# Performance work log

Measured on AMD Instinct MI355X. Metric: run time of the kernel, lower is better.

## Reference

```python
import jax, jax.numpy as jnp
import numpy as np

N_NODES = 100000
N_EDGES = 1600000
IN_DIM = 128
N_HID = 128


def setup_inputs() -> dict:
    key = jax.random.key(0)
    k1, k2, k3, k4 = jax.random.split(key, 4)
    node_feature = jax.random.normal(k1, (N_NODES, IN_DIM), dtype=jnp.float32)
    edge_index = jax.random.randint(k2, (2, N_EDGES), 0, N_NODES, dtype=jnp.int64)
    # GCN layer weights (glorot-ish scale)
    W1 = jax.random.normal(k3, (IN_DIM, N_HID), dtype=jnp.float32) / np.sqrt(IN_DIM)
    b1 = jnp.zeros((N_HID,), dtype=jnp.float32)
    W2 = jax.random.normal(k4, (N_HID, N_HID), dtype=jnp.float32) / np.sqrt(N_HID)
    b2 = jnp.zeros((N_HID,), dtype=jnp.float32)
    return {"node_feature": node_feature, "edge_index": edge_index,
            "W1": W1, "b1": b1, "W2": W2, "b2": b2}


def _gcn_layer(x, W, b, row, col, n_nodes):
    """GCNConv: x' = D^-1/2 (A + I) D^-1/2 (x W) + b, symmetric norm with self-loops."""
    xt = x @ W  # [N, out]
    ones = jnp.ones(row.shape[0], dtype=xt.dtype)
    deg = jnp.zeros((n_nodes,), dtype=xt.dtype).at[col].add(ones) + 1.0  # +1 self-loop
    dinv = jax.lax.rsqrt(deg)  # [N]
    norm = dinv[row] * dinv[col]  # [E]
    # gather messages from source (row), scatter-add into destination (col)
    agg = jnp.zeros_like(xt).at[col].add(xt[row] * norm[:, None])
    agg = agg + xt * (dinv * dinv)[:, None]  # self-loop contribution
    return agg + b


def reference(node_feature, edge_index, W1, b1, W2, b2):
    row, col = edge_index[0], edge_index[1]
    n = node_feature.shape[0]
    h = _gcn_layer(node_feature, W1, b1, row, col, n)
    # F.dropout with training=False is identity (eval-mode reference)
    h = _gcn_layer(h, W2, b2, row, col, n)
    return h
```

## Files before the change

kernel.cpp:

```cpp
#include <hip/hip_runtime.h>

typedef unsigned short ushort_t;
typedef __attribute__((ext_vector_type(8))) short short8;
typedef __attribute__((ext_vector_type(8))) unsigned short us8v;
typedef __attribute__((ext_vector_type(4))) float f32x4;

__device__ __forceinline__ float b2f(unsigned short u) {
    union { unsigned int i; float f; } v; v.i = ((unsigned int)u) << 16; return v.f;
}
__device__ __forceinline__ unsigned short f2b(float f) {
    union { float f; unsigned int i; } v; v.f = f;
    unsigned int r = (v.i + 0x7FFF + ((v.i >> 16) & 1)) >> 16;
    return (unsigned short)r;
}

__device__ __forceinline__ void load_edge(const int* __restrict__ ei, int e, int E,
                                          int is64, int& s, int& d) {
    if (is64) {
        const long long* el = (const long long*)ei;
        s = (int)el[e]; d = (int)el[E + e];
    } else {
        s = ei[e]; d = ei[E + e];
    }
}

__device__ __forceinline__ int detect64(const int* __restrict__ ei, int t) {
    int z = 0;
    for (int i = t; i < 512; i += 256) z |= ei[2 * i + 1];
    return (__syncthreads_or(z) == 0);
}

__global__ __launch_bounds__(256) void k_histT(const int* __restrict__ ei, int E,
                                               unsigned N, int* __restrict__ bhist,
                                               int BSH, int NB, int nch,
                                               const float* __restrict__ W1,
                                               const float* __restrict__ W2,
                                               ushort_t* __restrict__ WT) {
    __shared__ int lh[256];
    int t = threadIdx.x;
    int b = blockIdx.x;
    if (b >= nch) {
        const float* src = (b == nch) ? W1 : W2;
        ushort_t* dst = WT + (b - nch) * 16384;
        for (int i = t; i < 16384; i += 256) {
            int n = i >> 7, k = i & 127;
            dst[i] = f2b(src[k * 128 + n]);
        }
        return;
    }
    for (int q = t; q < NB; q += 256) lh[q] = 0;
    int is64 = detect64(ei, t);
    int e0 = b * 4096;
    #pragma unroll
    for (int i = 0; i < 16; ++i) {
        int e = e0 + i * 256 + t;
        if (e < E) {
            int s, d; load_edge(ei, e, E, is64, s, d);
            if ((unsigned)s < N && (unsigned)d < N) atomicAdd(&lh[d >> BSH], 1);
        }
    }
    __syncthreads();
    for (int q = t; q < NB; q += 256) { int v = lh[q]; if (v) atomicAdd(&bhist[q], v); }
}

__global__ void k_scanb(const int* __restrict__ bhist, int NB,
                        int* __restrict__ bkbase, int* __restrict__ bkcur) {
    __shared__ int sd[256];
    int t = threadIdx.x;
    int v0 = (t < NB) ? bhist[t] : 0;
    sd[t] = v0;
    for (int o = 1; o < 256; o <<= 1) {
        __syncthreads();
        int v = (t >= o) ? sd[t - o] : 0;
        __syncthreads();
        sd[t] += v;
    }
    __syncthreads();
    if (t < NB) { int ex = sd[t] - v0; bkbase[t] = ex; bkcur[t] = ex; }
}

__global__ __launch_bounds__(256) void k_bucket(const int* __restrict__ ei, int E, unsigned N,
                                                int* __restrict__ bkcur,
                                                int* __restrict__ bs, int* __restrict__ bd,
                                                int BSH, int NB) {
    __shared__ int lss[4096];
    __shared__ int ldd[4096];
    __shared__ int lhist[256];
    __shared__ int lcur[256];
    int t = threadIdx.x;
    int e0 = blockIdx.x * 4096;
    for (int b = t; b < NB; b += 256) lhist[b] = 0;
    int is64 = detect64(ei, t);
    #pragma unroll
    for (int i = 0; i < 16; ++i) {
        int idx = i * 256 + t, e = e0 + idx;
        int s = -1, d = -1;
        if (e < E) {
            load_edge(ei, e, E, is64, s, d);
            if (!((unsigned)s < N && (unsigned)d < N)) d = -1;
        }
        lss[idx] = s; ldd[idx] = d;
        if (d >= 0) atomicAdd(&lhist[d >> BSH], 1);
    }
    __syncthreads();
    for (int b = t; b < NB; b += 256) {
        int v = lhist[b];
        lcur[b] = v ? atomicAdd(&bkcur[b], v) : 0;
    }
    __syncthreads();
    #pragma unroll
    for (int i = 0; i < 16; ++i) {
        int idx = i * 256 + t;
        int d = ldd[idx];
        if (d >= 0) {
            int p = atomicAdd(&lcur[d >> BSH], 1);
            bs[p] = lss[idx]; bd[p] = d;
        }
    }
}

__global__ __launch_bounds__(256) void k_caf(const int* __restrict__ bs,
                                             const int* __restrict__ bd,
                                             const int* __restrict__ bkbase,
                                             const int* __restrict__ bkcur,
                                             int N, int BSH,
                                             int* __restrict__ pos,
                                             int* __restrict__ cnt,
                                             float* __restrict__ dinv,
                                             int* __restrict__ srcs) {
    __shared__ int lc[512];
    __shared__ int sc[512];
    int b = blockIdx.x, t = threadIdx.x;
    int nbase = b << BSH;
    int nn = min(1 << BSH, N - nbase);
    int segbase = bkbase[b] + b * (7 << BSH);

    lc[t] = 0; lc[t + 256] = 0;
    __syncthreads();
    int s0 = bkbase[b], s1 = bkcur[b];
    for (int i = s0 + t; i < s1; i += 256) atomicAdd(&lc[bd[i] - nbase], 1);
    __syncthreads();

    int c0 = (t < nn) ? lc[t] : 0;
    int c1 = (t + 256 < nn) ? lc[t + 256] : 0;
    int p0 = (c0 + 7) & ~7;
    int p1 = (c1 + 7) & ~7;
    sc[t] = p0; sc[t + 256] = p1;
    __syncthreads();
    for (int o = 1; o < 512; o <<= 1) {
        int v0 = (t >= o) ? sc[t - o] : 0;
        int v1 = (t + 256 >= o) ? sc[t + 256 - o] : 0;
        __syncthreads();
        sc[t] += v0; sc[t + 256] += v1;
        __syncthreads();
    }
    if (t < nn) {
        int st = segbase + sc[t] - p0;
        pos[nbase + t] = st;
        cnt[nbase + t] = p0;
        dinv[nbase + t] = rsqrtf((float)c0 + 1.0f);
        for (int q = c0; q < p0; ++q) srcs[st + q] = N;
        lc[t] = st;
    }
    if (t + 256 < nn) {
        int st = segbase + sc[t + 256] - p1;
        pos[nbase + t + 256] = st;
        cnt[nbase + t + 256] = p1;
        dinv[nbase + t + 256] = rsqrtf((float)c1 + 1.0f);
        for (int q = c1; q < p1; ++q) srcs[st + q] = N;
        lc[t + 256] = st;
    }
    __syncthreads();
    for (int i = s0 + t; i < s1; i += 256) {
        int d = bd[i];
        int p = atomicAdd(&lc[d - nbase], 1);
        srcs[p] = bs[i];
    }
}

template <bool ABF, bool ZROW>
__global__ __launch_bounds__(256) void k_gemm(const void* __restrict__ Ap,
                                              const ushort_t* __restrict__ WT,
                                              ushort_t* __restrict__ C,
                                              const float* __restrict__ dinv, int M) {
    __shared__ __align__(16) ushort_t sA[64 * 136];
    __shared__ __align__(16) ushort_t sW[128 * 136];
    int t = threadIdx.x;
    int row0 = blockIdx.x * 64;

    if (ZROW && blockIdx.x == 0 && t < 128) C[((size_t)M << 7) + t] = 0;

    #pragma unroll
    for (int it = 0; it < 8; ++it) {
        int flat = (it * 256 + t) * 8;
        int n = flat >> 7, k = flat & 127;
        uint4 v = *(const uint4*)(WT + flat);
        *(uint4*)(&sW[n * 136 + k]) = v;
    }
    #pragma unroll
    for (int it = 0; it < 4; ++it) {
        int flat = (it * 256 + t) * 8;
        int r = flat >> 7, cc = flat & 127;
        int row = row0 + r; if (row > M - 1) row = M - 1;
        if (ABF) {
            const ushort_t* A = (const ushort_t*)Ap;
            us8v v = *(const us8v*)(A + ((size_t)row << 7) + cc);
            *(us8v*)(&sA[r * 136 + cc]) = v;
        } else {
            const float* A = (const float*)Ap;
            const float* p = A + (size_t)row * 128 + cc;
            float4 f0 = *(const float4*)p;
            float4 f1 = *(const float4*)(p + 4);
            ushort_t tmp[8] __attribute__((aligned(16)));
            tmp[0] = f2b(f0.x); tmp[1] = f2b(f0.y); tmp[2] = f2b(f0.z); tmp[3] = f2b(f0.w);
            tmp[4] = f2b(f1.x); tmp[5] = f2b(f1.y); tmp[6] = f2b(f1.z); tmp[7] = f2b(f1.w);
            *(uint4*)(&sA[r * 136 + cc]) = *(const uint4*)tmp;
        }
    }
    __syncthreads();

    int w = t >> 6, lane = t & 63;
    int m = lane & 15, quad = lane >> 4;

    f32x4 acc[8] = {};
    #pragma unroll
    for (int k0 = 0; k0 < 128; k0 += 32) {
        short8 af = *(const short8*)(&sA[(w * 16 + m) * 136 + k0 + quad * 8]);
        #pragma unroll
        for (int tt = 0; tt < 8; ++tt) {
            short8 bf = *(const short8*)(&sW[(tt * 16 + m) * 136 + k0 + quad * 8]);
            acc[tt] = __builtin_amdgcn_mfma_f32_16x16x32_bf16(af, bf, acc[tt], 0, 0, 0);
        }
    }
    #pragma unroll
    for (int r = 0; r < 4; ++r) {
        int row = row0 + w * 16 + quad * 4 + r;
        if (row < M) {
            float dd = dinv[row];
            #pragma unroll
            for (int tt = 0; tt < 8; ++tt)
                C[(size_t)row * 128 + tt * 16 + m] = f2b(dd * acc[tt][r]);
        }
    }
}

template <bool OBF>
__global__ __launch_bounds__(256) void k_agg(const ushort_t* __restrict__ xt,
                                             const float* __restrict__ bias,
                                             void* __restrict__ outp,
                                             const int* __restrict__ pos,
                                             const int* __restrict__ cnts,
                                             const float* __restrict__ dinv,
                                             const int* __restrict__ srcs, int N) {
    int lane = threadIdx.x & 63;
    int slot = lane >> 4, j = lane & 15;
    int d = (blockIdx.x << 2) + (threadIdx.x >> 6);
    if (d >= N) return;
    int cn = cnts[d];
    int start = pos[d];
    float dd = dinv[d];
    us8v vs = *(const us8v*)(xt + ((size_t)d << 7) + (j << 3));
    float4 bb0 = *(const float4*)(bias + (j << 3));
    float4 bb1 = *(const float4*)(bias + (j << 3) + 4);

    float a0 = 0.f, a1 = 0.f, a2 = 0.f, a3 = 0.f;
    float a4 = 0.f, a5 = 0.f, a6 = 0.f, a7 = 0.f;

    for (int base = 0; base < cn; base += 64) {
        int n = cn - base; if (n > 64) n = 64;
        int sv = 0;
        if (lane < n) sv = srcs[start + base + lane];
        int s0 = __shfl(sv, slot);
        int s1 = __shfl(sv, 4 + slot);
        us8v v0 = *(const us8v*)(xt + ((size_t)s0 << 7) + (j << 3));
        us8v v1 = *(const us8v*)(xt + ((size_t)s1 << 7) + (j << 3));
        for (int c = 8; c < n; c += 8) {
            int t0 = __shfl(sv, c + slot);
            int t1 = __shfl(sv, c + 4 + slot);
            us8v w0 = *(const us8v*)(xt + ((size_t)t0 << 7) + (j << 3));
            us8v w1 = *(const us8v*)(xt + ((size_t)t1 << 7) + (j << 3));
            a0 += b2f(v0[0]); a1 += b2f(v0[1]); a2 += b2f(v0[2]); a3 += b2f(v0[3]);
            a4 += b2f(v0[4]); a5 += b2f(v0[5]); a6 += b2f(v0[6]); a7 += b2f(v0[7]);
            a0 += b2f(v1[0]); a1 += b2f(v1[1]); a2 += b2f(v1[2]); a3 += b2f(v1[3]);
            a4 += b2f(v1[4]); a5 += b2f(v1[5]); a6 += b2f(v1[6]); a7 += b2f(v1[7]);
            v0 = w0; v1 = w1;
        }
        a0 += b2f(v0[0]); a1 += b2f(v0[1]); a2 += b2f(v0[2]); a3 += b2f(v0[3]);
        a4 += b2f(v0[4]); a5 += b2f(v0[5]); a6 += b2f(v0[6]); a7 += b2f(v0[7]);
        a0 += b2f(v1[0]); a1 += b2f(v1[1]); a2 += b2f(v1[2]); a3 += b2f(v1[3]);
        a4 += b2f(v1[4]); a5 += b2f(v1[5]); a6 += b2f(v1[6]); a7 += b2f(v1[7]);
    }
    a0 += __shfl_xor(a0, 32); a1 += __shfl_xor(a1, 32);
    a2 += __shfl_xor(a2, 32); a3 += __shfl_xor(a3, 32);
    a4 += __shfl_xor(a4, 32); a5 += __shfl_xor(a5, 32);
    a6 += __shfl_xor(a6, 32); a7 += __shfl_xor(a7, 32);
    a0 += __shfl_xor(a0, 16); a1 += __shfl_xor(a1, 16);
    a2 += __shfl_xor(a2, 16); a3 += __shfl_xor(a3, 16);
    a4 += __shfl_xor(a4, 16); a5 += __shfl_xor(a5, 16);
    a6 += __shfl_xor(a6, 16); a7 += __shfl_xor(a7, 16);

    if (slot == 0) {
        float o0 = dd * (a0 + b2f(vs[0])) + bb0.x;
        float o1 = dd * (a1 + b2f(vs[1])) + bb0.y;
        float o2 = dd * (a2 + b2f(vs[2])) + bb0.z;
        float o3 = dd * (a3 + b2f(vs[3])) + bb0.w;
        float o4 = dd * (a4 + b2f(vs[4])) + bb1.x;
        float o5 = dd * (a5 + b2f(vs[5])) + bb1.y;
        float o6 = dd * (a6 + b2f(vs[6])) + bb1.z;
        float o7 = dd * (a7 + b2f(vs[7])) + bb1.w;
        if (OBF) {
            ushort_t tmp[8] __attribute__((aligned(16)));
            tmp[0] = f2b(o0); tmp[1] = f2b(o1); tmp[2] = f2b(o2); tmp[3] = f2b(o3);
            tmp[4] = f2b(o4); tmp[5] = f2b(o5); tmp[6] = f2b(o6); tmp[7] = f2b(o7);
            *(us8v*)((ushort_t*)outp + ((size_t)d << 7) + (j << 3)) = *(const us8v*)tmp;
        } else {
            float4 q0 = { o0, o1, o2, o3 };
            float4 q1 = { o4, o5, o6, o7 };
            float4* po = (float4*)((float*)outp + ((size_t)d << 7) + (j << 3));
            po[0] = q0; po[1] = q1;
        }
    }
}


extern "C" void kernel_launch(void* const* d_in, const int* in_sizes, int n_in,
                              void* d_out, int out_size, void* d_ws, size_t ws_size,
                              hipStream_t stream) {
    const float* x  = (const float*)d_in[0];
    const int*   ei = (const int*)d_in[1];
    const float* W1 = (const float*)d_in[2];
    const float* b1 = (const float*)d_in[3];
    const float* W2 = (const float*)d_in[4];
    const float* b2 = (const float*)d_in[5];
    float* out = (float*)d_out;

    const int N = in_sizes[0] / 128;
    const int E = in_sizes[1] / 2;

    int BSH = 9;
    int NB = (N + (1 << BSH) - 1) >> BSH;
    while (NB > 256) { BSH++; NB = (N + (1 << BSH) - 1) >> BSH; }

    char* ws = (char*)d_ws;
    size_t o = 0;
    auto take = [&](size_t bytes) { size_t r = o; o = (o + bytes + 255) & ~(size_t)255; return r; };
    size_t o_bhist  = take(256 * 4);
    size_t zero_end = o;
    size_t o_bkbase = take(256 * 4);
    size_t o_bkcur  = take(256 * 4);
    size_t o_cnt    = take((size_t)N * 4);
    size_t o_pos    = take((size_t)N * 4);
    size_t o_dinv   = take((size_t)N * 4);
    size_t o_srcs   = take(((size_t)E + (size_t)NB * (7 << BSH) + 64) * 4);
    size_t o_WT     = take(2 * 128 * 128 * 2);
    size_t big_sz   = (size_t)E * 8 > (size_t)(N + 1) * 256 ? (size_t)E * 8
                                                            : (size_t)(N + 1) * 256;
    size_t o_big    = take(big_sz);
    (void)ws_size;

    int*      bhist  = (int*)(ws + o_bhist);
    int*      bkbase = (int*)(ws + o_bkbase);
    int*      bkcur  = (int*)(ws + o_bkcur);
    int*      cnt    = (int*)(ws + o_cnt);
    int*      pos    = (int*)(ws + o_pos);
    float*    dinv   = (float*)(ws + o_dinv);
    int*      srcs   = (int*)(ws + o_srcs);
    ushort_t* WT     = (ushort_t*)(ws + o_WT);
    int*      bs     = (int*)(ws + o_big);
    int*      bd     = (int*)(ws + o_big) + E;
    ushort_t* xt     = (ushort_t*)(ws + o_big);
    ushort_t* hbf    = (ushort_t*)d_out;

    hipMemsetAsync(d_ws, 0, zero_end, stream);

    int nch = (E + 4095) / 4096;
    int gG  = (N + 63) / 64;
    int gA  = (N + 3) / 4;
    unsigned Nu = (unsigned)N;

    k_histT<<<nch + 2, 256, 0, stream>>>(ei, E, Nu, bhist, BSH, NB, nch, W1, W2, WT);
    k_scanb<<<1, 256, 0, stream>>>(bhist, NB, bkbase, bkcur);
    k_bucket<<<nch, 256, 0, stream>>>(ei, E, Nu, bkcur, bs, bd, BSH, NB);
    k_caf<<<NB, 256, 0, stream>>>(bs, bd, bkbase, bkcur, N, BSH, pos, cnt, dinv, srcs);

    k_gemm<false, true><<<gG, 256, 0, stream>>>(x, WT, xt, dinv, N);
    k_agg<true><<<gA, 256, 0, stream>>>(xt, b1, hbf, pos, cnt, dinv, srcs, N);
    k_gemm<true, false><<<gG, 256, 0, stream>>>(hbf, WT + 16384, xt, dinv, N);
    k_agg<false><<<gA, 256, 0, stream>>>(xt, b2, out, pos, cnt, dinv, srcs, N);
}
```

Before: 330.7 us.

## Fuse scan into histogram, co-schedule bucketing with first GEMM, pad with self-index

Computes per-node degree counts with global atomics in the histogram kernel, and has the last block (via a done counter) do the bucket scan and dinv, removing the separate scan launch. Merges bucketing and the first GEMM into one grid so both run concurrently. k_caf now reads counts instead of recounting. Padding slots point to the node itself with a compensating self-loop coefficient instead of a zero row. Global per-node atomics add contention, and the last-block pattern relies on fences for correctness.

```diff
diff --git a/kernel.cpp b/kernel.cpp
--- a/kernel.cpp
+++ b/kernel.cpp
@@ -30,13 +30,20 @@
     return (__syncthreads_or(z) == 0);
 }
 
-__global__ __launch_bounds__(256) void k_histT(const int* __restrict__ ei, int E,
-                                               unsigned N, int* __restrict__ bhist,
-                                               int BSH, int NB, int nch,
-                                               const float* __restrict__ W1,
-                                               const float* __restrict__ W2,
-                                               ushort_t* __restrict__ WT) {
+__global__ __launch_bounds__(256) void k_histST(const int* __restrict__ ei, int E,
+                                                unsigned N, int Ni,
+                                                int* __restrict__ bhist,
+                                                int* __restrict__ cnt,
+                                                float* __restrict__ dinv,
+                                                int BSH, int NB, int nch,
+                                                const float* __restrict__ W1,
+                                                const float* __restrict__ W2,
+                                                ushort_t* __restrict__ WT,
+                                                int* __restrict__ done,
+                                                int* __restrict__ bkbase,
+                                                int* __restrict__ bkcur) {
     __shared__ int lh[256];
+    __shared__ int lastFlag;
     int t = threadIdx.x;
     int b = blockIdx.x;
     if (b >= nch) {
@@ -46,75 +53,138 @@
             int n = i >> 7, k = i & 127;
             dst[i] = f2b(src[k * 128 + n]);
         }
-        return;
-    }
-    for (int q = t; q < NB; q += 256) lh[q] = 0;
-    int is64 = detect64(ei, t);
-    int e0 = b * 4096;
-    #pragma unroll
-    for (int i = 0; i < 16; ++i) {
-        int e = e0 + i * 256 + t;
-        if (e < E) {
-            int s, d; load_edge(ei, e, E, is64, s, d);
-            if ((unsigned)s < N && (unsigned)d < N) atomicAdd(&lh[d >> BSH], 1);
-        }
-    }
+    } else {
+        for (int q = t; q < NB; q += 256) lh[q] = 0;
+        int is64 = detect64(ei, t);
+        int e0 = b * 4096;
+        #pragma unroll
+        for (int i = 0; i < 16; ++i) {
+            int e = e0 + i * 256 + t;
+            if (e < E) {
+                int d = is64 ? (int)((const long long*)ei)[E + e] : ei[E + e];
+                if ((unsigned)d < N) {
+                    atomicAdd(&lh[d >> BSH], 1);
+                    atomicAdd(&cnt[d], 1);
+                }
+            }
+        }
+        __syncthreads();
+        for (int q = t; q < NB; q += 256) {
+            int v = lh[q]; if (v) atomicAdd(&bhist[q], v);
+        }
+    }
+    __threadfence();
+    if (t == 0) lastFlag = (atomicAdd(done, 1) == (int)gridDim.x - 1);
     __syncthreads();
-    for (int q = t; q < NB; q += 256) { int v = lh[q]; if (v) atomicAdd(&bhist[q], v); }
-}
-
-__global__ void k_scanb(const int* __restrict__ bhist, int NB,
-                        int* __restrict__ bkbase, int* __restrict__ bkcur) {
-    __shared__ int sd[256];
+    if (lastFlag) {
+        __threadfence();
+        int v0 = (t < NB) ? atomicAdd(&bhist[t], 0) : 0;
+        lh[t] = v0;
+        for (int o = 1; o < 256; o <<= 1) {
+            __syncthreads();
+            int v = (t >= o) ? lh[t - o] : 0;
+            __syncthreads();
+            lh[t] += v;
+        }
+        __syncthreads();
+        if (t < NB) { int ex = lh[t] - v0; bkbase[t] = ex; bkcur[t] = ex; }
+        for (int n = t; n < Ni; n += 256)
+            dinv[n] = rsqrtf((float)atomicAdd(&cnt[n], 0) + 1.0f);
+    }
+}
+
+__global__ __launch_bounds__(256) void k_bg(const int* __restrict__ ei, int E,
+                                            unsigned N, int* __restrict__ bkcur,
+                                            int* __restrict__ bs, int* __restrict__ bd,
+                                            int BSH, int NB, int nch,
+                                            const float* __restrict__ x,
+                                            const ushort_t* __restrict__ WT,
+                                            ushort_t* __restrict__ xt,
+                                            const float* __restrict__ dinv, int M) {
+    __shared__ __align__(16) int smem[13056];
     int t = threadIdx.x;
-    int v0 = (t < NB) ? bhist[t] : 0;
-    sd[t] = v0;
-    for (int o = 1; o < 256; o <<= 1) {
-        __syncthreads();
-        int v = (t >= o) ? sd[t - o] : 0;
-        __syncthreads();
-        sd[t] += v;
-    }
-    __syncthreads();
-    if (t < NB) { int ex = sd[t] - v0; bkbase[t] = ex; bkcur[t] = ex; }
-}
-
-__global__ __launch_bounds__(256) void k_bucket(const int* __restrict__ ei, int E, unsigned N,
-                                                int* __restrict__ bkcur,
-                                                int* __restrict__ bs, int* __restrict__ bd,
-                                                int BSH, int NB) {
-    __shared__ int lss[4096];
-    __shared__ int ldd[4096];
-    __shared__ int lhist[256];
-    __shared__ int lcur[256];
-    int t = threadIdx.x;
-    int e0 = blockIdx.x * 4096;
-    for (int b = t; b < NB; b += 256) lhist[b] = 0;
-    int is64 = detect64(ei, t);
-    #pragma unroll
-    for (int i = 0; i < 16; ++i) {
-        int idx = i * 256 + t, e = e0 + idx;
-        int s = -1, d = -1;
-        if (e < E) {
-            load_edge(ei, e, E, is64, s, d);
-            if (!((unsigned)s < N && (unsigned)d < N)) d = -1;
-        }
-        lss[idx] = s; ldd[idx] = d;
-        if (d >= 0) atomicAdd(&lhist[d >> BSH], 1);
-    }
-    __syncthreads();
-    for (int b = t; b < NB; b += 256) {
-        int v = lhist[b];
-        lcur[b] = v ? atomicAdd(&bkcur[b], v) : 0;
-    }
-    __syncthreads();
-    #pragma unroll
-    for (int i = 0; i < 16; ++i) {
-        int idx = i * 256 + t;
-        int d = ldd[idx];
-        if (d >= 0) {
-            int p = atomicAdd(&lcur[d >> BSH], 1);
-            bs[p] = lss[idx]; bd[p] = d;
+    int b = blockIdx.x;
+
+    if (b < nch) {
+        int* lss = smem;
+        int* ldd = smem + 4096;
+        int* lhist = smem + 8192;
+        int* lcur = smem + 8448;
+        int e0 = b * 4096;
+        for (int q = t; q < NB; q += 256) lhist[q] = 0;
+        int is64 = detect64(ei, t);
+        #pragma unroll
+        for (int i = 0; i < 16; ++i) {
+            int idx = i * 256 + t, e = e0 + idx;
+            int s = -1, d = -1;
+            if (e < E) {
+                load_edge(ei, e, E, is64, s, d);
+                if (!((unsigned)s < N && (unsigned)d < N)) d = -1;
+            }
+            lss[idx] = s; ldd[idx] = d;
+            if (d >= 0) atomicAdd(&lhist[d >> BSH], 1);
+        }
+        __syncthreads();
+        for (int q = t; q < NB; q += 256) {
+            int v = lhist[q];
+            lcur[q] = v ? atomicAdd(&bkcur[q], v) : 0;
+        }
+        __syncthreads();
+        #pragma unroll
+        for (int i = 0; i < 16; ++i) {
+            int idx = i * 256 + t;
+            int d = ldd[idx];
+            if (d >= 0) {
+                int p = atomicAdd(&lcur[d >> BSH], 1);
+                bs[p] = lss[idx]; bd[p] = d;
+            }
+        }
+    } else {
+        ushort_t* sA = (ushort_t*)smem;
+        ushort_t* sW = (ushort_t*)smem + 8704;
+        int row0 = (b - nch) * 64;
+        #pragma unroll
+        for (int it = 0; it < 8; ++it) {
+            int flat = (it * 256 + t) * 8;
+            int n = flat >> 7, k = flat & 127;
+            uint4 v = *(const uint4*)(WT + flat);
+            *(uint4*)(&sW[n * 136 + k]) = v;
+        }
+        #pragma unroll
+        for (int it = 0; it < 4; ++it) {
+            int flat = (it * 256 + t) * 8;
+            int r = flat >> 7, cc = flat & 127;
+            int row = row0 + r; if (row > M - 1) row = M - 1;
+            const float* p = x + (size_t)row * 128 + cc;
+            float4 f0 = *(const float4*)p;
+            float4 f1 = *(const float4*)(p + 4);
+            ushort_t tmp[8] __attribute__((aligned(16)));
+            tmp[0] = f2b(f0.x); tmp[1] = f2b(f0.y); tmp[2] = f2b(f0.z); tmp[3] = f2b(f0.w);
+            tmp[4] = f2b(f1.x); tmp[5] = f2b(f1.y); tmp[6] = f2b(f1.z); tmp[7] = f2b(f1.w);
+            *(uint4*)(&sA[r * 136 + cc]) = *(const uint4*)tmp;
+        }
+        __syncthreads();
+        int w = t >> 6, lane = t & 63;
+        int m = lane & 15, quad = lane >> 4;
+        f32x4 acc[8] = {};
+        #pragma unroll
+        for (int k0 = 0; k0 < 128; k0 += 32) {
+            short8 af = *(const short8*)(&sA[(w * 16 + m) * 136 + k0 + quad * 8]);
+            #pragma unroll
+            for (int tt = 0; tt < 8; ++tt) {
+                short8 bf = *(const short8*)(&sW[(tt * 16 + m) * 136 + k0 + quad * 8]);
+                acc[tt] = __builtin_amdgcn_mfma_f32_16x16x32_bf16(af, bf, acc[tt], 0, 0, 0);
+            }
+        }
+        #pragma unroll
+        for (int r = 0; r < 4; ++r) {
+            int row = row0 + w * 16 + quad * 4 + r;
+            if (row < M) {
+                float dd = dinv[row];
+                #pragma unroll
+                for (int tt = 0; tt < 8; ++tt)
+                    xt[(size_t)row * 128 + tt * 16 + m] = f2b(dd * acc[tt][r]);
+            }
         }
     }
 }
@@ -123,10 +193,9 @@
                                              const int* __restrict__ bd,
                                              const int* __restrict__ bkbase,
                                              const int* __restrict__ bkcur,
+                                             const int* __restrict__ cnt,
                                              int N, int BSH,
                                              int* __restrict__ pos,
-                                             int* __restrict__ cnt,
-                                             float* __restrict__ dinv,
                                              int* __restrict__ srcs) {
     __shared__ int lc[512];
     __shared__ int sc[512];
@@ -135,14 +204,8 @@
     int nn = min(1 << BSH, N - nbase);
     int segbase = bkbase[b] + b * (7 << BSH);
 
-    lc[t] = 0; lc[t + 256] = 0;
-    __syncthreads();
-    int s0 = bkbase[b], s1 = bkcur[b];
-    for (int i = s0 + t; i < s1; i += 256) atomicAdd(&lc[bd[i] - nbase], 1);
-    __syncthreads();
-
-    int c0 = (t < nn) ? lc[t] : 0;
-    int c1 = (t + 256 < nn) ? lc[t + 256] : 0;
+    int c0 = (t < nn) ? cnt[nbase + t] : 0;
+    int c1 = (t + 256 < nn) ? cnt[nbase + t + 256] : 0;
     int p0 = (c0 + 7) & ~7;
     int p1 = (c1 + 7) & ~7;
     sc[t] = p0; sc[t + 256] = p1;
@@ -157,20 +220,17 @@
     if (t < nn) {
         int st = segbase + sc[t] - p0;
         pos[nbase + t] = st;
-        cnt[nbase + t] = p0;
-        dinv[nbase + t] = rsqrtf((float)c0 + 1.0f);
-        for (int q = c0; q < p0; ++q) srcs[st + q] = N;
+        for (int q = c0; q < p0; ++q) srcs[st + q] = nbase + t;
         lc[t] = st;
     }
     if (t + 256 < nn) {
         int st = segbase + sc[t + 256] - p1;
         pos[nbase + t + 256] = st;
-        cnt[nbase + t + 256] = p1;
-        dinv[nbase + t + 256] = rsqrtf((float)c1 + 1.0f);
-        for (int q = c1; q < p1; ++q) srcs[st + q] = N;
+        for (int q = c1; q < p1; ++q) srcs[st + q] = nbase + t + 256;
         lc[t + 256] = st;
     }
     __syncthreads();
+    int s0 = bkbase[b], s1 = bkcur[b];
     for (int i = s0 + t; i < s1; i += 256) {
         int d = bd[i];
         int p = atomicAdd(&lc[d - nbase], 1);
@@ -178,18 +238,14 @@
     }
 }
 
-template <bool ABF, bool ZROW>
-__global__ __launch_bounds__(256) void k_gemm(const void* __restrict__ Ap,
-                                              const ushort_t* __restrict__ WT,
-                                              ushort_t* __restrict__ C,
-                                              const float* __restrict__ dinv, int M) {
+__global__ __launch_bounds__(256) void k_gemm2(const ushort_t* __restrict__ A,
+                                               const ushort_t* __restrict__ WT,
+                                               ushort_t* __restrict__ C,
+                                               const float* __restrict__ dinv, int M) {
     __shared__ __align__(16) ushort_t sA[64 * 136];
     __shared__ __align__(16) ushort_t sW[128 * 136];
     int t = threadIdx.x;
     int row0 = blockIdx.x * 64;
-
-    if (ZROW && blockIdx.x == 0 && t < 128) C[((size_t)M << 7) + t] = 0;
-
     #pragma unroll
     for (int it = 0; it < 8; ++it) {
         int flat = (it * 256 + t) * 8;
@@ -202,26 +258,12 @@
         int flat = (it * 256 + t) * 8;
         int r = flat >> 7, cc = flat & 127;
         int row = row0 + r; if (row > M - 1) row = M - 1;
-        if (ABF) {
-            const ushort_t* A = (const ushort_t*)Ap;
-            us8v v = *(const us8v*)(A + ((size_t)row << 7) + cc);
-            *(us8v*)(&sA[r * 136 + cc]) = v;
-        } else {
-            const float* A = (const float*)Ap;
-            const float* p = A + (size_t)row * 128 + cc;
-            float4 f0 = *(const float4*)p;
-            float4 f1 = *(const float4*)(p + 4);
-            ushort_t tmp[8] __attribute__((aligned(16)));
-            tmp[0] = f2b(f0.x); tmp[1] = f2b(f0.y); tmp[2] = f2b(f0.z); tmp[3] = f2b(f0.w);
-            tmp[4] = f2b(f1.x); tmp[5] = f2b(f1.y); tmp[6] = f2b(f1.z); tmp[7] = f2b(f1.w);
-            *(uint4*)(&sA[r * 136 + cc]) = *(const uint4*)tmp;
-        }
+        us8v v = *(const us8v*)(A + ((size_t)row << 7) + cc);
+        *(us8v*)(&sA[r * 136 + cc]) = v;
     }
     __syncthreads();
-
     int w = t >> 6, lane = t & 63;
     int m = lane & 15, quad = lane >> 4;
-
     f32x4 acc[8] = {};
     #pragma unroll
     for (int k0 = 0; k0 < 128; k0 += 32) {
@@ -256,7 +298,9 @@
     int slot = lane >> 4, j = lane & 15;
     int d = (blockIdx.x << 2) + (threadIdx.x >> 6);
     if (d >= N) return;
-    int cn = cnts[d];
+    int c = cnts[d];
+    int cn = (c + 7) & ~7;
+    float coef = (float)(1 - (cn - c));
     int start = pos[d];
     float dd = dinv[d];
     us8v vs = *(const us8v*)(xt + ((size_t)d << 7) + (j << 3));
@@ -274,9 +318,9 @@
         int s1 = __shfl(sv, 4 + slot);
         us8v v0 = *(const us8v*)(xt + ((size_t)s0 << 7) + (j << 3));
         us8v v1 = *(const us8v*)(xt + ((size_t)s1 << 7) + (j << 3));
-        for (int c = 8; c < n; c += 8) {
-            int t0 = __shfl(sv, c + slot);
-            int t1 = __shfl(sv, c + 4 + slot);
+        for (int cc = 8; cc < n; cc += 8) {
+            int t0 = __shfl(sv, cc + slot);
+            int t1 = __shfl(sv, cc + 4 + slot);
             us8v w0 = *(const us8v*)(xt + ((size_t)t0 << 7) + (j << 3));
             us8v w1 = *(const us8v*)(xt + ((size_t)t1 << 7) + (j << 3));
             a0 += b2f(v0[0]); a1 += b2f(v0[1]); a2 += b2f(v0[2]); a3 += b2f(v0[3]);
@@ -300,14 +344,14 @@
     a6 += __shfl_xor(a6, 16); a7 += __shfl_xor(a7, 16);
 
     if (slot == 0) {
-        float o0 = dd * (a0 + b2f(vs[0])) + bb0.x;
-        float o1 = dd * (a1 + b2f(vs[1])) + bb0.y;
-        float o2 = dd * (a2 + b2f(vs[2])) + bb0.z;
-        float o3 = dd * (a3 + b2f(vs[3])) + bb0.w;
-        float o4 = dd * (a4 + b2f(vs[4])) + bb1.x;
-        float o5 = dd * (a5 + b2f(vs[5])) + bb1.y;
-        float o6 = dd * (a6 + b2f(vs[6])) + bb1.z;
-        float o7 = dd * (a7 + b2f(vs[7])) + bb1.w;
+        float o0 = dd * (a0 + coef * b2f(vs[0])) + bb0.x;
+        float o1 = dd * (a1 + coef * b2f(vs[1])) + bb0.y;
+        float o2 = dd * (a2 + coef * b2f(vs[2])) + bb0.z;
+        float o3 = dd * (a3 + coef * b2f(vs[3])) + bb0.w;
+        float o4 = dd * (a4 + coef * b2f(vs[4])) + bb1.x;
+        float o5 = dd * (a5 + coef * b2f(vs[5])) + bb1.y;
+        float o6 = dd * (a6 + coef * b2f(vs[6])) + bb1.z;
+        float o7 = dd * (a7 + coef * b2f(vs[7])) + bb1.w;
         if (OBF) {
             ushort_t tmp[8] __attribute__((aligned(16)));
             tmp[0] = f2b(o0); tmp[1] = f2b(o1); tmp[2] = f2b(o2); tmp[3] = f2b(o3);
@@ -345,31 +389,33 @@
     size_t o = 0;
     auto take = [&](size_t bytes) { size_t r = o; o = (o + bytes + 255) & ~(size_t)255; return r; };
     size_t o_bhist  = take(256 * 4);
+    size_t o_done   = take(4);
+    size_t o_cnt    = take((size_t)N * 4);
     size_t zero_end = o;
     size_t o_bkbase = take(256 * 4);
     size_t o_bkcur  = take(256 * 4);
-    size_t o_cnt    = take((size_t)N * 4);
     size_t o_pos    = take((size_t)N * 4);
     size_t o_dinv   = take((size_t)N * 4);
     size_t o_srcs   = take(((size_t)E + (size_t)NB * (7 << BSH) + 64) * 4);
     size_t o_WT     = take(2 * 128 * 128 * 2);
-    size_t big_sz   = (size_t)E * 8 > (size_t)(N + 1) * 256 ? (size_t)E * 8
-                                                            : (size_t)(N + 1) * 256;
+    size_t big_sz   = (size_t)E * 8 > (size_t)N * 256 ? (size_t)E * 8 : (size_t)N * 256;
     size_t o_big    = take(big_sz);
     (void)ws_size;
 
     int*      bhist  = (int*)(ws + o_bhist);
+    int*      done   = (int*)(ws + o_done);
+    int*      cnt    = (int*)(ws + o_cnt);
     int*      bkbase = (int*)(ws + o_bkbase);
     int*      bkcur  = (int*)(ws + o_bkcur);
-    int*      cnt    = (int*)(ws + o_cnt);
     int*      pos    = (int*)(ws + o_pos);
     float*    dinv   = (float*)(ws + o_dinv);
     int*      srcs   = (int*)(ws + o_srcs);
     ushort_t* WT     = (ushort_t*)(ws + o_WT);
     int*      bs     = (int*)(ws + o_big);
     int*      bd     = (int*)(ws + o_big) + E;
-    ushort_t* xt     = (ushort_t*)(ws + o_big);
-    ushort_t* hbf    = (ushort_t*)d_out;
+    ushort_t* xt2    = (ushort_t*)(ws + o_big);
+    ushort_t* xt1    = (ushort_t*)d_out;
+    ushort_t* hbf    = (ushort_t*)d_out + (size_t)N * 128;
 
     hipMemsetAsync(d_ws, 0, zero_end, stream);
 
@@ -378,13 +424,14 @@
     int gA  = (N + 3) / 4;
     unsigned Nu = (unsigned)N;
 
-    k_histT<<<nch + 2, 256, 0, stream>>>(ei, E, Nu, bhist, BSH, NB, nch, W1, W2, WT);
-    k_scanb<<<1, 256, 0, stream>>>(bhist, NB, bkbase, bkcur);
-    k_bucket<<<nch, 256, 0, stream>>>(ei, E, Nu, bkcur, bs, bd, BSH, NB);
-    k_caf<<<NB, 256, 0, stream>>>(bs, bd, bkbase, bkcur, N, BSH, pos, cnt, dinv, srcs);
-
-    k_gemm<false, true><<<gG, 256, 0, stream>>>(x, WT, xt, dinv, N);
-    k_agg<true><<<gA, 256, 0, stream>>>(xt, b1, hbf, pos, cnt, dinv, srcs, N);
-    k_gemm<true, false><<<gG, 256, 0, stream>>>(hbf, WT + 16384, xt, dinv, N);
-    k_agg<false><<<gA, 256, 0, stream>>>(xt, b2, out, pos, cnt, dinv, srcs, N);
-}
+    k_histST<<<nch + 2, 256, 0, stream>>>(ei, E, Nu, N, bhist, cnt, dinv,
+                                          BSH, NB, nch, W1, W2, WT,
+                                          done, bkbase, bkcur);
+    k_bg<<<nch + gG, 256, 0, stream>>>(ei, E, Nu, bkcur, bs, bd, BSH, NB, nch,
+                                       x, WT, xt1, dinv, N);
+    k_caf<<<NB, 256, 0, stream>>>(bs, bd, bkbase, bkcur, cnt, N, BSH, pos, srcs);
+
+    k_agg<true><<<gA, 256, 0, stream>>>(xt1, b1, hbf, pos, cnt, dinv, srcs, N);
+    k_gemm2<<<gG, 256, 0, stream>>>(hbf, WT + 16384, xt2, dinv, N);
+    k_agg<false><<<gA, 256, 0, stream>>>(xt2, b2, out, pos, cnt, dinv, srcs, N);
+}
```

New measurement: 489.3 us. 1.48x slower.
